# Optimization experiments

Measured on AMD Instinct MI355X. Metric: run time of the kernel, lower is better.

## Reference

```python
import jax, jax.numpy as jnp
import numpy as np

N = 30000      # total atoms in batch
E = 60000      # directed bonds
FIN = 64       # raw atom feature dim (in_channels)
H = 768        # hidden_channels
G = 600        # number of graphs
L = 20         # seq_length
NL = 3         # num_layers
EA = 6         # edge_attr dim (hard-coded: Linear(in_channels + 6, ...))
EPS = 1e-5     # BatchNorm eps


def _bn(x, g, b, m, v):
    # eval-mode BatchNorm1d with running stats
    return (x - m) * jax.lax.rsqrt(v + EPS) * g + b


def setup_inputs() -> dict:
    key = jax.random.key(0)
    ks = list(jax.random.split(key, 48))
    kit = iter(ks)

    def rn(shp, s=0.02):
        return jax.random.normal(next(kit), shp, jnp.float32) * s

    def bn_params(shape_prefix=()):
        g = jax.random.uniform(next(kit), shape_prefix + (H,), jnp.float32, 0.5, 1.5)
        b = rn(shape_prefix + (H,), 0.1)
        m = rn(shape_prefix + (H,), 0.1)
        v = jax.random.uniform(next(kit), shape_prefix + (H,), jnp.float32, 0.5, 1.5)
        return g, b, m, v

    inp = {}
    inp["x"] = jax.random.normal(next(kit), (N, FIN), jnp.float32)
    inp["edge_index"] = jax.random.randint(next(kit), (2, E), 0, N)
    inp["edge_attr"] = jax.random.uniform(next(kit), (E, EA), jnp.float32)
    inp["batch_idx"] = jnp.sort(jax.random.randint(next(kit), (N,), 0, G))
    inp["num_graphs"] = G

    # input_mlp
    inp["W_in"] = rn((FIN, H)); inp["b_in"] = rn((H,))
    inp["bn0_g"], inp["bn0_b"], inp["bn0_m"], inp["bn0_v"] = bn_params()
    # stacked WLNConv layers
    inp["Wc"] = rn((NL, H + EA, H)); inp["bc"] = rn((NL, H))
    inp["bnc_g"], inp["bnc_b"], inp["bnc_m"], inp["bnc_v"] = bn_params((NL,))
    # sequence_proj
    inp["Ws"] = rn((3 * H, H)); inp["bs"] = rn((H,))
    inp["bns_g"], inp["bns_b"], inp["bns_m"], inp["bns_v"] = bn_params()
    # pooler
    inp["Wp"] = rn((H, H)); inp["bp"] = rn((H,))
    # node_decoder
    inp["Wd1"] = rn((H, H)); inp["bd1"] = rn((H,))
    inp["bnd_g"], inp["bnd_b"], inp["bnd_m"], inp["bnd_v"] = bn_params()
    inp["Wd2"] = rn((H, FIN)); inp["bd2"] = rn((FIN,))
    return inp


def reference(x, edge_index, edge_attr, batch_idx, num_graphs,
              W_in, b_in, bn0_g, bn0_b, bn0_m, bn0_v,
              Wc, bc, bnc_g, bnc_b, bnc_m, bnc_v,
              Ws, bs, bns_g, bns_b, bns_m, bns_v,
              Wp, bp,
              Wd1, bd1, bnd_g, bnd_b, bnd_m, bnd_v,
              Wd2, bd2):
    n = x.shape[0]
    # input_mlp (eval: dropout = identity)
    h = _bn(jnp.maximum(x @ W_in + b_in, 0.0), bn0_g, bn0_b, bn0_m, bn0_v)

    # add self loops once (same edge list for every conv layer)
    loops = jnp.arange(n)
    src = jnp.concatenate([edge_index[0], loops])            # [E+N]
    dst = jnp.concatenate([edge_index[1], loops])            # [E+N]
    ea = jnp.concatenate(
        [edge_attr, jnp.zeros((n, edge_attr.shape[1]), edge_attr.dtype)], axis=0)

    total = h
    for i in range(Wc.shape[0]):
        # message: gather x_j, concat edge_attr, linear + relu
        m_in = jnp.concatenate([h[src], ea], axis=1)          # [E+N, H+6]
        msg = jnp.maximum(m_in @ Wc[i] + bc[i], 0.0)          # [E+N, H]
        # aggregate: scatter-add into target nodes
        agg = jax.ops.segment_sum(msg, dst, num_segments=n)   # [N, H]
        h = _bn(agg, bnc_g[i], bnc_b[i], bnc_m[i], bnc_v[i])
        total = total + h                                     # sum over layer outputs

    # global pools per graph
    counts = jax.ops.segment_sum(jnp.ones((n,), total.dtype), batch_idx,
                                 num_segments=num_graphs)     # [G]
    x_add = jax.ops.segment_sum(total, batch_idx, num_segments=num_graphs)
    x_mean = x_add / jnp.maximum(counts, 1.0)[:, None]
    x_max = jax.ops.segment_max(total, batch_idx, num_segments=num_graphs)
    x_max = jnp.where(counts[:, None] > 0, x_max, 0.0)

    comb = jnp.concatenate([x_mean, x_add, x_max], axis=1)    # [G, 3H]
    hs = _bn(jnp.maximum(comb @ Ws + bs, 0.0), bns_g, bns_b, bns_m, bns_v)

    last_hidden = jnp.broadcast_to(hs[:, None, :], (hs.shape[0], L, hs.shape[1]))
    pooler = jnp.tanh(hs @ Wp + bp)                           # [G, H]

    # expand graph embedding back to nodes (batch_idx is sorted -> gather)
    z = pooler[batch_idx]                                     # [N, H]
    d = _bn(jnp.maximum(z @ Wd1 + bd1, 0.0), bnd_g, bnd_b, bnd_m, bnd_v)
    recon = d @ Wd2 + bd2                                     # [N, FIN]
    return last_hidden, pooler, recon
```

## Files before the change

kernel.cpp:

```cpp
#include <hip/hip_runtime.h>

#define NATOMS 30000
#define NPAD   30080
#define NEDGE  60000
#define HDIM   768
#define H4     192
#define NG     600
#define GPAD   640
#define LSEQ   20
#define BNEPS  1e-5f

typedef __attribute__((ext_vector_type(8))) short bf16x8;
typedef __attribute__((ext_vector_type(4))) float f32x4;

__device__ __forceinline__ ushort f2bf(float f) {
    union { float f; unsigned u; } v; v.f = f;
    unsigned r = v.u + 0x7FFFu + ((v.u >> 16) & 1u);
    return (ushort)(r >> 16);
}
__device__ __forceinline__ float bf2f(ushort u) {
    union { unsigned u; float f; } v; v.u = ((unsigned)u) << 16; return v.f;
}
__device__ __forceinline__ ushort4 pack4(float4 v) {
    ushort4 r; r.x = f2bf(v.x); r.y = f2bf(v.y); r.z = f2bf(v.z); r.w = f2bf(v.w); return r;
}
__device__ __forceinline__ float4 unpack4(ushort4 u) {
    float4 r; r.x = bf2f(u.x); r.y = bf2f(u.y); r.z = bf2f(u.z); r.w = bf2f(u.w); return r;
}
__device__ __forceinline__ void gl_lds16(const ushort* g, ushort* l) {
    __builtin_amdgcn_global_load_lds(
        (const __attribute__((address_space(1))) void*)(g),
        (__attribute__((address_space(3))) void*)(l), 16, 0, 0);
}

#define PC0 (3L*768*768)
#define PC1 (PC0 + 768L*64)
#define PC2 (PC1 + 768L*2304)
#define PC3 (PC2 + 768L*768)
#define PC4 (PC3 + 768L*768)
#define PC5 (PC4 + 128L*768)
#define PC6 (PC5 + 480000L)
#define PC7 (PC6 + NATOMS)
__global__ __launch_bounds__(256) void prep_k(
    const float* __restrict__ Wc, const float* __restrict__ Win, const float* __restrict__ Ws,
    const float* __restrict__ Wp, const float* __restrict__ Wd1, const float* __restrict__ Wd2,
    const float* __restrict__ x,
    ushort* __restrict__ WTc, ushort* __restrict__ WinT, ushort* __restrict__ WsT,
    ushort* __restrict__ WpT, ushort* __restrict__ Wd1T, ushort* __restrict__ Wd2T,
    ushort* __restrict__ XB, int* __restrict__ cnt)
{
    long idx = (long)blockIdx.x * 256 + threadIdx.x;
    if (idx < PC0) {
        long b = idx / (768 * 768), rem = idx % (768 * 768);
        long n = rem / 768, k = rem % 768;
        WTc[idx] = f2bf(Wc[b * 594432 + k * 768 + n]);
    } else if (idx < PC1) {
        long j = idx - PC0; long n = j / 64, k = j % 64;
        WinT[j] = f2bf(Win[k * 768 + n]);
    } else if (idx < PC2) {
        long j = idx - PC1; long n = j / 2304, k = j % 2304;
        WsT[j] = f2bf(Ws[k * 768 + n]);
    } else if (idx < PC3) {
        long j = idx - PC2; long n = j / 768, k = j % 768;
        WpT[j] = f2bf(Wp[k * 768 + n]);
    } else if (idx < PC4) {
        long j = idx - PC3; long n = j / 768, k = j % 768;
        Wd1T[j] = f2bf(Wd1[k * 768 + n]);
    } else if (idx < PC5) {
        long j = idx - PC4; long n = j / 768, k = j % 768;
        Wd2T[j] = (n < 64) ? f2bf(Wd2[k * 64 + n]) : (ushort)0;
    } else if (idx < PC6) {
        long j = idx - PC5;
        ((ushort4*)XB)[j] = pack4(((const float4*)x)[j]);
    } else if (idx < PC7) {
        cnt[idx - PC6] = 0;
    }
}

template <int EPI, int SWZ>
__global__ __launch_bounds__(256) void gemm_bt(
    const ushort* __restrict__ A, const ushort* __restrict__ Bt,
    float* __restrict__ Cf, ushort* __restrict__ Cb, ushort* __restrict__ Cb2,
    const float* __restrict__ bias,
    const float* __restrict__ bng, const float* __restrict__ bnb,
    const float* __restrict__ bnm, const float* __restrict__ bnv,
    int Mreal, int Nreal, int K, int nbx)
{
    __shared__ ushort As[128 * 32];
    __shared__ ushort Bs[128 * 32];
    int t = threadIdx.x;
    int lane = t & 63, wave = t >> 6;
    int wr = wave >> 1, wc = wave & 1;
    int brow, bcol;
    if (SWZ) {
        int nwg = gridDim.x;
        int q = nwg >> 3, r = nwg & 7;
        int id = blockIdx.x;
        int xcd = id & 7, i = id >> 3;
        int s = (xcd < r) ? xcd * (q + 1) + i : r * (q + 1) + (xcd - r) * q + i;
        bcol = s % 6; brow = s / 6;
    } else {
        bcol = blockIdx.x; brow = blockIdx.y;
    }

    f32x4 acc[4][4];
    #pragma unroll
    for (int i = 0; i < 4; i++)
        #pragma unroll
        for (int j = 0; j < 4; j++) acc[i][j] = (f32x4)0.f;

    const int r0 = wave * 32 + (lane >> 2);
    const int ce = (lane & 3) * 8;
    const ushort* Ag0 = A + (size_t)(brow * 128 + r0) * K + ce;
    const ushort* Ag1 = A + (size_t)(brow * 128 + r0 + 16) * K + ce;
    const ushort* Bg0 = Bt + (size_t)(bcol * 128 + r0) * K + ce;
    const ushort* Bg1 = Bt + (size_t)(bcol * 128 + r0 + 16) * K + ce;
    ushort* Al0 = As + wave * 1024;
    ushort* Al1 = As + wave * 1024 + 512;
    ushort* Bl0 = Bs + wave * 1024;
    ushort* Bl1 = Bs + wave * 1024 + 512;

    const int lr = lane & 15, lk = (lane >> 4) * 8;

    for (int kt = 0; kt < K; kt += 32) {
        __syncthreads();
        gl_lds16(Ag0 + kt, Al0);
        gl_lds16(Ag1 + kt, Al1);
        gl_lds16(Bg0 + kt, Bl0);
        gl_lds16(Bg1 + kt, Bl1);
        __syncthreads();

        bf16x8 af[4], bfr[4];
        #pragma unroll
        for (int mf = 0; mf < 4; mf++)
            af[mf] = *(const bf16x8*)(&As[(wr * 64 + mf * 16 + lr) * 32 + lk]);
        #pragma unroll
        for (int nf = 0; nf < 4; nf++)
            bfr[nf] = *(const bf16x8*)(&Bs[(wc * 64 + nf * 16 + lr) * 32 + lk]);
        #pragma unroll
        for (int mf = 0; mf < 4; mf++)
            #pragma unroll
            for (int nf = 0; nf < 4; nf++)
                acc[mf][nf] = __builtin_amdgcn_mfma_f32_16x16x32_bf16(af[mf], bfr[nf], acc[mf][nf], 0, 0, 0);
    }

    const int lq = lane >> 4;
    #pragma unroll
    for (int mf = 0; mf < 4; mf++) {
        #pragma unroll
        for (int nf = 0; nf < 4; nf++) {
            int col = bcol * 128 + wc * 64 + nf * 16 + lr;
            #pragma unroll
            for (int rg = 0; rg < 4; rg++) {
                int row = brow * 128 + wr * 64 + mf * 16 + lq * 4 + rg;
                if (row < Mreal && col < Nreal) {
                    float v = acc[mf][nf][rg];
                    if (EPI >= 1) v += bias[col];
                    if (EPI == 1) {
                        v = fmaxf(v, 0.f);
                        float s = bng[col] * rsqrtf(bnv[col] + BNEPS);
                        v = (v - bnm[col]) * s + bnb[col];
                    } else if (EPI == 2) {
                        v = tanhf(v);
                    }
                    size_t o = (size_t)row * Nreal + col;
                    if (Cf) Cf[o] = v;
                    if (Cb) Cb[o] = f2bf(v);
                    if (Cb2) Cb2[o] = f2bf(v);
                }
            }
        }
    }
}


__global__ void count_k(const int* __restrict__ dst_a, int* __restrict__ cnt)
{
    int e = blockIdx.x * 256 + threadIdx.x;
    if (e < NEDGE) atomicAdd(&cnt[dst_a[e]], 1);
}

__global__ __launch_bounds__(1024) void scan_k(const int* __restrict__ cnt,
                                               int* __restrict__ row_off,
                                               int* __restrict__ cur)
{
    __shared__ int part[1024];
    const int CH = (NATOMS + 1023) / 1024;
    int t = threadIdx.x;
    int base = t * CH;
    int s = 0;
    for (int i = base; i < base + CH && i < NATOMS; i++) s += cnt[i];
    part[t] = s;
    __syncthreads();
    for (int off = 1; off < 1024; off <<= 1) {
        int v = (t >= off) ? part[t - off] : 0;
        __syncthreads();
        part[t] += v;
        __syncthreads();
    }
    int excl = part[t] - s;
    for (int i = base; i < base + CH && i < NATOMS; i++) {
        row_off[i] = excl;
        cur[i] = excl;
        excl += cnt[i];
    }
    if (t == 1023) row_off[NATOMS] = part[1023];
}

__global__ void fill_k(const int* __restrict__ src_a, const int* __restrict__ dst_a,
                       const float* __restrict__ ea,
                       int* __restrict__ cur, int* __restrict__ srcs, float* __restrict__ eas)
{
    int e = blockIdx.x * 256 + threadIdx.x;
    if (e >= NEDGE) return;
    int d = dst_a[e];
    int pos = atomicAdd(&cur[d], 1);
    srcs[pos] = src_a[e];
    float* o = eas + (size_t)pos * 8;
    o[0] = ea[e * 6 + 0]; o[1] = ea[e * 6 + 1]; o[2] = ea[e * 6 + 2];
    o[3] = ea[e * 6 + 3]; o[4] = ea[e * 6 + 4]; o[5] = ea[e * 6 + 5];
}

#define NPN 4
__global__ __launch_bounds__(192) void node_agg_k(
    const ushort* __restrict__ P, const int* __restrict__ row_off,
    const int* __restrict__ srcs, const float* __restrict__ eas,
    const float* __restrict__ Wce, const float* __restrict__ bc,
    const float* __restrict__ g, const float* __restrict__ b,
    const float* __restrict__ m, const float* __restrict__ vv,
    ushort* __restrict__ TOTAL, ushort* __restrict__ HB)
{
    int n0 = blockIdx.x * NPN;
    int c4 = threadIdx.x;
    const float4* W4 = (const float4*)Wce;
    float4 w0 = W4[0 * H4 + c4], w1 = W4[1 * H4 + c4], w2 = W4[2 * H4 + c4];
    float4 w3 = W4[3 * H4 + c4], w4 = W4[4 * H4 + c4], w5 = W4[5 * H4 + c4];
    float4 bb = ((const float4*)bc)[c4];
    float4 gg = ((const float4*)g)[c4], bo = ((const float4*)b)[c4];
    float4 mm = ((const float4*)m)[c4], vq = ((const float4*)vv)[c4];
    float4 sc;
    sc.x = gg.x * rsqrtf(vq.x + BNEPS); sc.y = gg.y * rsqrtf(vq.y + BNEPS);
    sc.z = gg.z * rsqrtf(vq.z + BNEPS); sc.w = gg.w * rsqrtf(vq.w + BNEPS);

    for (int u = 0; u < NPN; u++) {
        int n = n0 + u;
        if (n >= NATOMS) return;
        float4 p = unpack4(((const ushort4*)P)[(size_t)n * H4 + c4]);
        float4 acc;
        acc.x = fmaxf(p.x + bb.x, 0.f); acc.y = fmaxf(p.y + bb.y, 0.f);
        acc.z = fmaxf(p.z + bb.z, 0.f); acc.w = fmaxf(p.w + bb.w, 0.f);

        int lo = row_off[n], hi = row_off[n + 1];
        for (int j = lo; j < hi; j++) {
            int s = srcs[j];
            const float* e8 = eas + (size_t)j * 8;
            float4 eA = *(const float4*)(e8);
            float e4v = e8[4], e5v = e8[5];
            float4 ps = unpack4(((const ushort4*)P)[(size_t)s * H4 + c4]);
            float4 v;
            v.x = fmaxf(ps.x + eA.x * w0.x + eA.y * w1.x + eA.z * w2.x + eA.w * w3.x + e4v * w4.x + e5v * w5.x + bb.x, 0.f);
            v.y = fmaxf(ps.y + eA.x * w0.y + eA.y * w1.y + eA.z * w2.y + eA.w * w3.y + e4v * w4.y + e5v * w5.y + bb.y, 0.f);
            v.z = fmaxf(ps.z + eA.x * w0.z + eA.y * w1.z + eA.z * w2.z + eA.w * w3.z + e4v * w4.z + e5v * w5.z + bb.z, 0.f);
            v.w = fmaxf(ps.w + eA.x * w0.w + eA.y * w1.w + eA.z * w2.w + eA.w * w3.w + e4v * w4.w + e5v * w5.w + bb.w, 0.f);
            acc.x += v.x; acc.y += v.y; acc.z += v.z; acc.w += v.w;
        }

        float4 hv;
        hv.x = (acc.x - mm.x) * sc.x + bo.x;
        hv.y = (acc.y - mm.y) * sc.y + bo.y;
        hv.z = (acc.z - mm.z) * sc.z + bo.z;
        hv.w = (acc.w - mm.w) * sc.w + bo.w;
        size_t idx = (size_t)n * H4 + c4;
        float4 tt = unpack4(((const ushort4*)TOTAL)[idx]);
        tt.x += hv.x; tt.y += hv.y; tt.z += hv.z; tt.w += hv.w;
        ((ushort4*)TOTAL)[idx] = pack4(tt);
        ((ushort4*)HB)[idx] = pack4(hv);
    }
}

__global__ __launch_bounds__(64) void pool_k(const ushort* __restrict__ TOTAL,
                                             const int* __restrict__ bidx,
                                             ushort* __restrict__ COMB)
{
    int g = blockIdx.x;
    int c4 = blockIdx.y * 64 + threadIdx.x;
    ushort4* C4 = (ushort4*)COMB;
    int lo, hi;
    { int a = 0, b = NATOMS; while (a < b) { int mid = (a + b) >> 1; if (bidx[mid] < g) a = mid + 1; else b = mid; } lo = a; }
    { int a = lo, b = NATOMS; while (a < b) { int mid = (a + b) >> 1; if (bidx[mid] <= g) a = mid + 1; else b = mid; } hi = a; }
    int cnt = hi - lo;
    float4 sum = {0.f, 0.f, 0.f, 0.f};
    float4 mx = {-INFINITY, -INFINITY, -INFINITY, -INFINITY};
    for (int r = lo; r < hi; r++) {
        float4 v = unpack4(((const ushort4*)TOTAL)[(size_t)r * H4 + c4]);
        sum.x += v.x; sum.y += v.y; sum.z += v.z; sum.w += v.w;
        mx.x = fmaxf(mx.x, v.x); mx.y = fmaxf(mx.y, v.y);
        mx.z = fmaxf(mx.z, v.z); mx.w = fmaxf(mx.w, v.w);
    }
    float inv = 1.f / fmaxf((float)cnt, 1.f);
    if (cnt == 0) { mx.x = mx.y = mx.z = mx.w = 0.f; }
    float4 mean = {sum.x * inv, sum.y * inv, sum.z * inv, sum.w * inv};
    C4[(size_t)g * 576 + c4] = pack4(mean);
    C4[(size_t)g * 576 + 192 + c4] = pack4(sum);
    C4[(size_t)g * 576 + 384 + c4] = pack4(mx);
}

__global__ void bcast_k(const float* __restrict__ HS, float* __restrict__ out0)
{
    size_t idx = (size_t)blockIdx.x * 256 + threadIdx.x;
    int c4 = (int)(idx % H4);
    int g = (int)(idx / ((size_t)H4 * LSEQ));
    ((float4*)out0)[idx] = ((const float4*)HS)[(size_t)g * H4 + c4];
}

__global__ void recon_k(const float* __restrict__ RG, const int* __restrict__ bidx,
                        float* __restrict__ out2)
{
    size_t idx = (size_t)blockIdx.x * 256 + threadIdx.x;
    int n = (int)(idx >> 4), c4 = (int)(idx & 15);
    ((float4*)out2)[idx] = ((const float4*)RG)[(size_t)bidx[n] * 16 + c4];
}

extern "C" void kernel_launch(void* const* d_in, const int* in_sizes, int n_in,
                              void* d_out, int out_size, void* d_ws, size_t ws_size,
                              hipStream_t stream)
{
    const float* x    = (const float*)d_in[0];
    const int*   ei   = (const int*)d_in[1];
    const float* ea   = (const float*)d_in[2];
    const int*   bidx = (const int*)d_in[3];
    const float* Win  = (const float*)d_in[5];
    const float* bin  = (const float*)d_in[6];
    const float* bn0g = (const float*)d_in[7];
    const float* bn0b = (const float*)d_in[8];
    const float* bn0m = (const float*)d_in[9];
    const float* bn0v = (const float*)d_in[10];
    const float* Wc   = (const float*)d_in[11];
    const float* bc   = (const float*)d_in[12];
    const float* bncg = (const float*)d_in[13];
    const float* bncb = (const float*)d_in[14];
    const float* bncm = (const float*)d_in[15];
    const float* bncv = (const float*)d_in[16];
    const float* Ws   = (const float*)d_in[17];
    const float* bs   = (const float*)d_in[18];
    const float* bnsg = (const float*)d_in[19];
    const float* bnsb = (const float*)d_in[20];
    const float* bnsm = (const float*)d_in[21];
    const float* bnsv = (const float*)d_in[22];
    const float* Wp   = (const float*)d_in[23];
    const float* bp   = (const float*)d_in[24];
    const float* Wd1  = (const float*)d_in[25];
    const float* bd1  = (const float*)d_in[26];
    const float* bndg = (const float*)d_in[27];
    const float* bndb = (const float*)d_in[28];
    const float* bndm = (const float*)d_in[29];
    const float* bndv = (const float*)d_in[30];
    const float* Wd2  = (const float*)d_in[31];
    const float* bd2  = (const float*)d_in[32];

    float* out  = (float*)d_out;
    float* out0 = out;
    float* out1 = out + (size_t)NG * LSEQ * HDIM;
    float* out2 = out1 + (size_t)NG * HDIM;

    char* w = (char*)d_ws;
    size_t off = 0;
    auto alloc = [&](size_t bytes) { void* p = w + off; off += (bytes + 255) & ~255ULL; return p; };
    ushort* P      = (ushort*)alloc((size_t)NPAD * HDIM * 2);
    ushort* TOTAL  = (ushort*)alloc((size_t)NATOMS * HDIM * 2);
    ushort* HB     = (ushort*)alloc((size_t)NPAD * HDIM * 2);
    ushort* XB     = (ushort*)alloc((size_t)NPAD * 64 * 2);
    ushort* WTc    = (ushort*)alloc((size_t)3 * 768 * 768 * 2);
    ushort* WinT   = (ushort*)alloc((size_t)768 * 64 * 2);
    ushort* WsT    = (ushort*)alloc((size_t)768 * 2304 * 2);
    ushort* WpT    = (ushort*)alloc((size_t)768 * 768 * 2);
    ushort* Wd1T   = (ushort*)alloc((size_t)768 * 768 * 2);
    ushort* Wd2T   = (ushort*)alloc((size_t)128 * 768 * 2);
    ushort* COMB   = (ushort*)alloc((size_t)GPAD * 2304 * 2);
    float*  HS     = (float*) alloc((size_t)NG * HDIM * 4);
    ushort* HSB    = (ushort*)alloc((size_t)GPAD * HDIM * 2);
    ushort* POOLB  = (ushort*)alloc((size_t)GPAD * HDIM * 2);
    ushort* DGB    = (ushort*)alloc((size_t)GPAD * HDIM * 2);
    float*  RECONG = (float*) alloc((size_t)NG * 64 * 4);
    int*    cnt    = (int*)   alloc((size_t)NATOMS * 4);
    int*    row_off= (int*)   alloc((size_t)(NATOMS + 1) * 4);
    int*    cur    = (int*)   alloc((size_t)NATOMS * 4);
    int*    srcs   = (int*)   alloc((size_t)NEDGE * 4);
    float*  eas    = (float*) alloc((size_t)NEDGE * 8 * 4);

    const int* src_a = ei;
    const int* dst_a = ei + NEDGE;

    prep_k<<<(int)((PC7 + 255) / 256), 256, 0, stream>>>(
        Wc, Win, Ws, Wp, Wd1, Wd2, x, WTc, WinT, WsT, WpT, Wd1T, Wd2T, XB, cnt);

    count_k<<<(NEDGE + 255) / 256, 256, 0, stream>>>(dst_a, cnt);
    scan_k<<<1, 1024, 0, stream>>>(cnt, row_off, cur);
    fill_k<<<(NEDGE + 255) / 256, 256, 0, stream>>>(src_a, dst_a, ea, cur, srcs, eas);

    gemm_bt<1, 1><<<1410, 256, 0, stream>>>(
        XB, WinT, nullptr, HB, TOTAL, bin, bn0g, bn0b, bn0m, bn0v, NATOMS, HDIM, 64, 6);

    for (int i = 0; i < 3; i++) {
        const float* Wcei = Wc + (size_t)i * 774 * HDIM + (size_t)HDIM * HDIM;
        const float* bci  = bc + i * HDIM;
        gemm_bt<0, 1><<<1410, 256, 0, stream>>>(
            HB, WTc + (size_t)i * 768 * 768, nullptr, P, nullptr,
            nullptr, nullptr, nullptr, nullptr, nullptr, NATOMS, HDIM, HDIM, 6);
        node_agg_k<<<(NATOMS + NPN - 1) / NPN, 192, 0, stream>>>(
            P, row_off, srcs, eas, Wcei, bci,
            bncg + i * HDIM, bncb + i * HDIM, bncm + i * HDIM, bncv + i * HDIM, TOTAL, HB);
    }

    pool_k<<<dim3(NG, 3), 64, 0, stream>>>(TOTAL, bidx, COMB);

    gemm_bt<1, 0><<<dim3(6, 5), 256, 0, stream>>>(
        COMB, WsT, HS, HSB, nullptr, bs, bnsg, bnsb, bnsm, bnsv, NG, HDIM, 2304, 6);

    bcast_k<<<(NG * LSEQ * H4) / 256, 256, 0, stream>>>(HS, out0);

    gemm_bt<2, 0><<<dim3(6, 5), 256, 0, stream>>>(
        HSB, WpT, out1, POOLB, nullptr, bp, nullptr, nullptr, nullptr, nullptr, NG, HDIM, HDIM, 6);

    gemm_bt<1, 0><<<dim3(6, 5), 256, 0, stream>>>(
        POOLB, Wd1T, nullptr, DGB, nullptr, bd1, bndg, bndb, bndm, bndv, NG, HDIM, HDIM, 6);

    gemm_bt<3, 0><<<dim3(1, 5), 256, 0, stream>>>(
        DGB, Wd2T, RECONG, nullptr, nullptr, bd2, nullptr, nullptr, nullptr, nullptr, NG, 64, HDIM, 1);

    recon_k<<<(NATOMS * 16) / 256, 256, 0, stream>>>(RECONG, bidx, out2);
}
```

Before: 804.9 us.

## Double-buffer LDS tiles in bf16 GEMM and raise nodes per aggregation block

The GEMM kernel now keeps two LDS buffers and issues the global-to-LDS loads for the next K tile before running the MFMAs on the current one, with one barrier per iteration instead of two. This aims to hide global load latency behind matrix math. The cost is double the LDS footprint, which may lower occupancy. Separately, the node aggregation kernel handles 8 nodes per block instead of 4, so each block's per-thread weight and BN setup is spread over more nodes.

Result: faster. 771.7 us (-4.1%).

```diff
diff --git a/kernel.cpp b/kernel.cpp
--- a/kernel.cpp
+++ b/kernel.cpp
@@ -86,8 +86,8 @@
     const float* __restrict__ bnm, const float* __restrict__ bnv,
     int Mreal, int Nreal, int K, int nbx)
 {
-    __shared__ ushort As[128 * 32];
-    __shared__ ushort Bs[128 * 32];
+    __shared__ ushort As[2][128 * 32];
+    __shared__ ushort Bs[2][128 * 32];
     int t = threadIdx.x;
     int lane = t & 63, wave = t >> 6;
     int wr = wave >> 1, wc = wave & 1;
@@ -115,33 +115,41 @@
     const ushort* Ag1 = A + (size_t)(brow * 128 + r0 + 16) * K + ce;
     const ushort* Bg0 = Bt + (size_t)(bcol * 128 + r0) * K + ce;
     const ushort* Bg1 = Bt + (size_t)(bcol * 128 + r0 + 16) * K + ce;
-    ushort* Al0 = As + wave * 1024;
-    ushort* Al1 = As + wave * 1024 + 512;
-    ushort* Bl0 = Bs + wave * 1024;
-    ushort* Bl1 = Bs + wave * 1024 + 512;
+    const int wo = wave * 1024;
 
     const int lr = lane & 15, lk = (lane >> 4) * 8;
 
+    gl_lds16(Ag0, &As[0][wo]);
+    gl_lds16(Ag1, &As[0][wo + 512]);
+    gl_lds16(Bg0, &Bs[0][wo]);
+    gl_lds16(Bg1, &Bs[0][wo + 512]);
+    __syncthreads();
+
+    int cur = 0;
     for (int kt = 0; kt < K; kt += 32) {
-        __syncthreads();
-        gl_lds16(Ag0 + kt, Al0);
-        gl_lds16(Ag1 + kt, Al1);
-        gl_lds16(Bg0 + kt, Bl0);
-        gl_lds16(Bg1 + kt, Bl1);
-        __syncthreads();
+        if (kt + 32 < K) {
+            int nb = cur ^ 1;
+            gl_lds16(Ag0 + kt + 32, &As[nb][wo]);
+            gl_lds16(Ag1 + kt + 32, &As[nb][wo + 512]);
+            gl_lds16(Bg0 + kt + 32, &Bs[nb][wo]);
+            gl_lds16(Bg1 + kt + 32, &Bs[nb][wo + 512]);
+        }
 
         bf16x8 af[4], bfr[4];
         #pragma unroll
         for (int mf = 0; mf < 4; mf++)
-            af[mf] = *(const bf16x8*)(&As[(wr * 64 + mf * 16 + lr) * 32 + lk]);
+            af[mf] = *(const bf16x8*)(&As[cur][(wr * 64 + mf * 16 + lr) * 32 + lk]);
         #pragma unroll
         for (int nf = 0; nf < 4; nf++)
-            bfr[nf] = *(const bf16x8*)(&Bs[(wc * 64 + nf * 16 + lr) * 32 + lk]);
+            bfr[nf] = *(const bf16x8*)(&Bs[cur][(wc * 64 + nf * 16 + lr) * 32 + lk]);
         #pragma unroll
         for (int mf = 0; mf < 4; mf++)
             #pragma unroll
             for (int nf = 0; nf < 4; nf++)
                 acc[mf][nf] = __builtin_amdgcn_mfma_f32_16x16x32_bf16(af[mf], bfr[nf], acc[mf][nf], 0, 0, 0);
+
+        __syncthreads();
+        cur ^= 1;
     }
 
     const int lq = lane >> 4;
@@ -221,7 +229,7 @@
     o[3] = ea[e * 6 + 3]; o[4] = ea[e * 6 + 4]; o[5] = ea[e * 6 + 5];
 }
 
-#define NPN 4
+#define NPN 8
 __global__ __launch_bounds__(192) void node_agg_k(
     const ushort* __restrict__ P, const int* __restrict__ row_off,
     const int* __restrict__ srcs, const float* __restrict__ eas,
```
